# Kernel optimization log

Measured on AMD Instinct MI355X. Metric: run time of the kernel, lower is better.

The kernel has to match this reference:

```python
import jax, jax.numpy as jnp
import numpy as np

NEG_INF = -9e15  # matches torch's -9000000000000000.0 mask value


def setup_inputs() -> dict:
    key = jax.random.key(0)
    k1, k2, k3, k4 = jax.random.split(key, 4)
    B, F_in, T, N, F_out = 8, 64, 12, 512, 64
    inp = {
        "input": jax.random.normal(k1, (B, F_in, T, N), dtype=jnp.float32),
        "adj": jax.random.randint(k2, (B, T, N, N), 0, 2, dtype=jnp.int32),
        "W": jax.random.normal(k3, (F_in, F_out), dtype=jnp.float32),
        "a": jax.random.normal(k4, (2 * F_out, 1), dtype=jnp.float32),
    }
    return inp


def reference(input, adj, W, a):
    # input: [B, F_in, T, N], adj: [B, T, N, N]
    F_out = W.shape[1]
    x = jnp.transpose(input, (0, 2, 3, 1))          # [B, T, N, F_in]
    Wh = jnp.einsum('btnf,fo->btno', x, W)          # [B, T, N, F_out]
    # score decomposition: e[i,j] = leakyrelu(a1.Wh_i + a2.Wh_j)
    a1 = a[:F_out, 0]
    a2 = a[F_out:, 0]
    f1 = Wh @ a1                                    # [B, T, N]
    f2 = Wh @ a2                                    # [B, T, N]
    e = jax.nn.leaky_relu(f1[..., :, None] + f2[..., None, :], 0.2)
    e = jnp.where(adj > 0, e, NEG_INF)
    attn = jax.nn.softmax(e, axis=-1)               # [B, T, N, N]
    h = jnp.einsum('btij,btjo->btio', attn, Wh)     # [B, T, N, F_out]
    return jax.nn.elu(h)                            # concat=True -> elu
```

## Files before the change

kernel.cpp:

```cpp
#include <hip/hip_runtime.h>
#include <hip/hip_bf16.h>

typedef float fx4 __attribute__((ext_vector_type(4)));
typedef short i16x8 __attribute__((ext_vector_type(8)));
typedef unsigned short u16;

#define NEG_INF_F (-9.0e15f)

__device__ inline u16 f2bf(float v){
  __hip_bfloat16 h = __float2bfloat16(v);
  return *reinterpret_cast<u16*>(&h);
}

__global__ __launch_bounds__(256) void gat_prep(
    const float* __restrict__ input,
    const float* __restrict__ W,
    const float* __restrict__ Avec,
    u16*   __restrict__ whB,
    float* __restrict__ f1w,
    float* __restrict__ f2w)
{
  __shared__ float Wl[64*64];
  __shared__ float Al[128];
  __shared__ u16   Rp[16384];
  const int tid = threadIdx.x;
  const int bt  = blockIdx.y;
  const int b   = bt / 12, t = bt % 12;
  const int xb  = blockIdx.x;
  const int n   = xb * 256 + tid;

  {
    const fx4* src = (const fx4*)W;
    fx4* dst = (fx4*)Wl;
    #pragma unroll
    for (int i = 0; i < 4; ++i) dst[tid + 256*i] = src[tid + 256*i];
    if (tid < 32) ((fx4*)Al)[tid] = ((const fx4*)Avec)[tid];
  }
  __syncthreads();

  const float* xp = input + ((size_t)b*64*12 + t) * 512 + n;

  fx4 acc[16];
  #pragma unroll
  for (int i = 0; i < 16; ++i) acc[i] = (fx4){0.f,0.f,0.f,0.f};

  #pragma unroll 8
  for (int f = 0; f < 64; ++f) {
    float xv = xp[(size_t)f * 6144];
    const fx4* wr = (const fx4*)(Wl + f*64);
    #pragma unroll
    for (int o4 = 0; o4 < 16; ++o4) acc[o4] += xv * wr[o4];
  }

  float s1 = 0.f, s2 = 0.f;
  #pragma unroll
  for (int o4 = 0; o4 < 16; ++o4) {
    fx4 v  = acc[o4];
    fx4 w1 = ((const fx4*)Al)[o4];
    fx4 w2 = ((const fx4*)Al)[o4 + 16];
    s1 += v[0]*w1[0] + v[1]*w1[1] + v[2]*w1[2] + v[3]*w1[3];
    s2 += v[0]*w2[0] + v[1]*w2[1] + v[2]*w2[2] + v[3]*w2[3];
  }
  f1w[bt*512 + n] = s1;
  f2w[bt*512 + n] = s2;

  const int ktl  = (n >> 5) & 7;
  const int q    = (n >> 3) & 3;
  const int e    = n & 7;
  const int rowb = ktl*2048 + q*128 + e;
  #pragma unroll
  for (int o4 = 0; o4 < 16; ++o4) {
    #pragma unroll
    for (int c = 0; c < 4; ++c) {
      const int o = o4*4 + c;
      Rp[rowb + (o >> 4)*512 + (o & 15)*8] = f2bf(acc[o4][c]);
    }
  }
  __syncthreads();

  uint4* dst = (uint4*)(whB + ((size_t)bt*16 + xb*8) * 2048);
  const uint4* src = (const uint4*)Rp;
  #pragma unroll
  for (int i = 0; i < 8; ++i) dst[tid + 256*i] = src[tid + 256*i];
}

__global__ __launch_bounds__(256, 4) void gat_attn(
    const int*   __restrict__ adj,
    const u16*   __restrict__ whB,
    const float* __restrict__ f1w,
    const float* __restrict__ f2w,
    float*       __restrict__ out)
{
  __shared__ float f2l[512];
  __shared__ float f1l[16];
  __shared__ float wmax[4];
  __shared__ float sums[16];
  __shared__ u16   attnl[16*512];

  const int tid = threadIdx.x;
  const int l   = tid & 63;
  const int w   = tid >> 6;
  const int bt  = blockIdx.y;
  const int it  = blockIdx.x;

  float2 fv = ((const float2*)(f2w + bt*512))[tid];
  ((float2*)f2l)[tid] = fv;
  float m2 = fmaxf(fv.x, fv.y);
  #pragma unroll
  for (int off = 32; off >= 1; off >>= 1) m2 = fmaxf(m2, __shfl_xor(m2, off));
  if (l == 0) wmax[w] = m2;
  if (tid < 16) f1l[tid] = f1w[bt*512 + it*16 + tid];
  __syncthreads();
  const float F2max = fmaxf(fmaxf(wmax[0], wmax[1]), fmaxf(wmax[2], wmax[3]));

  const fx4 f20 = ((const fx4*)f2l)[l];
  const fx4 f21 = ((const fx4*)f2l)[64 + l];
  fx4 v0, v1, vh0, vh1;
  #pragma unroll
  for (int c = 0; c < 4; ++c) {
    v0[c]  = __expf(f20[c] - F2max);
    v1[c]  = __expf(f21[c] - F2max);
    vh0[c] = __expf(0.2f*(f20[c] - F2max));
    vh1[c] = __expf(0.2f*(f21[c] - F2max));
  }

  const int R0     = w * 4;
  const int row_g0 = it*16 + R0;
  const int4* adj4 = (const int4*)(adj + (size_t)bt*512*512);

  int4 pre[2][2];
  #pragma unroll
  for (int p = 0; p < 2; ++p) {
    const int4* ar = adj4 + (size_t)(row_g0 + p) * 128;
    pre[p][0] = ar[l];
    pre[p][1] = ar[64 + l];
  }

  float ssum[4];
  #pragma unroll
  for (int r = 0; r < 4; ++r) {
    const int4 c0 = pre[r & 1][0];
    const int4 c1 = pre[r & 1][1];
    if (r + 2 < 4) {
      const int4* ar = adj4 + (size_t)(row_g0 + r + 2) * 128;
      pre[r & 1][0] = ar[l];
      pre[r & 1][1] = ar[64 + l];
    }
    const float f1v = f1l[R0 + r];

    float mx = NEG_INF_F;
    mx = fmaxf(mx, (c0.x > 0) ? f20[0] : NEG_INF_F);
    mx = fmaxf(mx, (c0.y > 0) ? f20[1] : NEG_INF_F);
    mx = fmaxf(mx, (c0.z > 0) ? f20[2] : NEG_INF_F);
    mx = fmaxf(mx, (c0.w > 0) ? f20[3] : NEG_INF_F);
    mx = fmaxf(mx, (c1.x > 0) ? f21[0] : NEG_INF_F);
    mx = fmaxf(mx, (c1.y > 0) ? f21[1] : NEG_INF_F);
    mx = fmaxf(mx, (c1.z > 0) ? f21[2] : NEG_INF_F);
    mx = fmaxf(mx, (c1.w > 0) ? f21[3] : NEG_INF_F);
    #pragma unroll
    for (int off = 32; off >= 1; off >>= 1) mx = fmaxf(mx, __shfl_xor(mx, off));

    const float tM = f1v + mx;
    const float M  = fmaxf(tM, 0.2f*tM);
    const float gap = F2max - mx;

    float sum = 0.f;
    ushort4 pk0, pk1;
    if (gap <= 80.f) {
      const float u  = __expf(f1v + F2max - M);
      const float uh = __expf(0.2f*(f1v + F2max) - M);
      const float thr = -f1v;
      float pv;
#define GAT_F(pkf, cc, ff, vv, vvh) { \
      const bool cpos = (ff) > thr; \
      float a = cpos ? (vv) : (vvh); \
      float bb = cpos ? u : uh; \
      pv = ((cc) > 0) ? a*bb : 0.f; sum += pv; pkf = f2bf(pv); }
      GAT_F(pk0.x, c0.x, f20[0], v0[0], vh0[0])
      GAT_F(pk0.y, c0.y, f20[1], v0[1], vh0[1])
      GAT_F(pk0.z, c0.z, f20[2], v0[2], vh0[2])
      GAT_F(pk0.w, c0.w, f20[3], v0[3], vh0[3])
      GAT_F(pk1.x, c1.x, f21[0], v1[0], vh1[0])
      GAT_F(pk1.y, c1.y, f21[1], v1[1], vh1[1])
      GAT_F(pk1.z, c1.z, f21[2], v1[2], vh1[2])
      GAT_F(pk1.w, c1.w, f21[3], v1[3], vh1[3])
#undef GAT_F
    } else {
      const float Mf = (mx == NEG_INF_F) ? NEG_INF_F : M;
      float pv;
#define GAT_S(pkf, cc, ff) { float s = f1v + (ff); float lr = fmaxf(s, 0.2f*s); \
      float ee = ((cc) > 0) ? lr : NEG_INF_F; \
      pv = __expf(ee - Mf); sum += pv; pkf = f2bf(pv); }
      GAT_S(pk0.x, c0.x, f20[0]) GAT_S(pk0.y, c0.y, f20[1])
      GAT_S(pk0.z, c0.z, f20[2]) GAT_S(pk0.w, c0.w, f20[3])
      GAT_S(pk1.x, c1.x, f21[0]) GAT_S(pk1.y, c1.y, f21[1])
      GAT_S(pk1.z, c1.z, f21[2]) GAT_S(pk1.w, c1.w, f21[3])
#undef GAT_S
    }
    ssum[r] = sum;

    const int rowR = R0 + r;
    const unsigned swz = (unsigned)((rowR & 7) << 4);
    char* base = (char*)attnl + rowR * 1024;
    *(ushort4*)(base + (((unsigned)(      8*l)) ^ swz)) = pk0;
    *(ushort4*)(base + (((unsigned)(512 + 8*l)) ^ swz)) = pk1;
  }

  #pragma unroll
  for (int r = 0; r < 4; ++r) {
    #pragma unroll
    for (int off = 32; off >= 1; off >>= 1) ssum[r] += __shfl_xor(ssum[r], off);
  }
  if (l == 0) {
    #pragma unroll
    for (int r = 0; r < 4; ++r) sums[R0 + r] = ssum[r];
  }
  __syncthreads();

  const int r = l & 15, q = l >> 4;
  const int ct = w;
  const unsigned swzB = (unsigned)((r & 7) << 4);
  const char* aBase = (const char*)attnl + r * 1024;
  const u16*  wp    = whB + (size_t)bt*32768 + ct*512 + l*8;
  fx4 acc = {0,0,0,0};

  #pragma unroll
  for (int kt = 0; kt < 16; ++kt) {
    i16x8 af = *(const i16x8*)(aBase + (((unsigned)(kt*64 + q*16)) ^ swzB));
    i16x8 bf = *(const i16x8*)(wp + kt*2048);
    acc = __builtin_amdgcn_mfma_f32_16x16x32_bf16(af, bf, acc, 0, 0, 0);
  }

  float* op = out + ((size_t)bt*512 + it*16) * 64;
  #pragma unroll
  for (int rr = 0; rr < 4; ++rr) {
    const float rs = 1.0f / sums[q*4 + rr];
    float v = acc[rr] * rs;
    v = v > 0.f ? v : expm1f(v);
    op[(q*4 + rr)*64 + ct*16 + r] = v;
  }
}

extern "C" void kernel_launch(void* const* d_in, const int* in_sizes, int n_in,
                              void* d_out, int out_size, void* d_ws, size_t ws_size,
                              hipStream_t stream) {
  const float* input = (const float*)d_in[0];
  const int*   adj   = (const int*)  d_in[1];
  const float* W     = (const float*)d_in[2];
  const float* Avec  = (const float*)d_in[3];
  float* out = (float*)d_out;

  char* ws = (char*)d_ws;
  u16*   whB = (u16*)ws;
  float* f1w = (float*)(ws + 6291456);
  float* f2w = (float*)(ws + 6291456 + 196608);

  gat_prep<<<dim3(2, 96), 256, 0, stream>>>(input, W, Avec, whB, f1w, f2w);
  gat_attn<<<dim3(32, 96), 256, 0, stream>>>(adj, whB, f1w, f2w, out);
}
```

Before: 50.62 us.

## Process two 16-row tiles per block with early adj prefetch and XCD-aware remap

Each attention block now covers 32 rows as two 16-row tiles. All adjacency loads for the first tile are issued at kernel start, before the f2 reduction. The second tile's adjacency is prefetched while the first tile's MFMA phase runs. A flat 1536-block grid is remapped so consecutive block ids spread across the 8 XCDs while neighbouring tiles of the same batch/time slice stay together. This halves per-block setup (f2 load, max, exp tables) and is meant to hide adj latency, at the cost of more registers and fewer blocks in flight.

```diff
diff --git a/kernel.cpp b/kernel.cpp
--- a/kernel.cpp
+++ b/kernel.cpp
@@ -92,26 +92,41 @@
     float*       __restrict__ out)
 {
   __shared__ float f2l[512];
-  __shared__ float f1l[16];
-  __shared__ float wmax[4];
-  __shared__ float sums[16];
+  __shared__ float f1l[32];
+  __shared__ float wmaxl[4];
+  __shared__ float sums[2][16];
   __shared__ u16   attnl[16*512];
 
   const int tid = threadIdx.x;
   const int l   = tid & 63;
   const int w   = tid >> 6;
-  const int bt  = blockIdx.y;
-  const int it  = blockIdx.x;
+
+  const int id  = blockIdx.x;
+  const int sid = (id & 7) * 192 + (id >> 3);
+  const int bt  = sid >> 4;
+  const int it  = sid & 15;
+
+  const int4* adj4 = (const int4*)(adj + (size_t)bt*512*512);
+
+  const int grow0 = it*32 + w*4;
+  int4 p0[4][2];
+  #pragma unroll
+  for (int r = 0; r < 4; ++r) {
+    const int4* ar = adj4 + (size_t)(grow0 + r) * 128;
+    p0[r][0] = ar[l];
+    p0[r][1] = ar[64 + l];
+  }
+  __builtin_amdgcn_sched_barrier(0);
 
   float2 fv = ((const float2*)(f2w + bt*512))[tid];
   ((float2*)f2l)[tid] = fv;
   float m2 = fmaxf(fv.x, fv.y);
   #pragma unroll
   for (int off = 32; off >= 1; off >>= 1) m2 = fmaxf(m2, __shfl_xor(m2, off));
-  if (l == 0) wmax[w] = m2;
-  if (tid < 16) f1l[tid] = f1w[bt*512 + it*16 + tid];
-  __syncthreads();
-  const float F2max = fmaxf(fmaxf(wmax[0], wmax[1]), fmaxf(wmax[2], wmax[3]));
+  if (l == 0) wmaxl[w] = m2;
+  if (tid < 32) f1l[tid] = f1w[bt*512 + it*32 + tid];
+  __syncthreads();
+  const float F2max = fmaxf(fmaxf(wmaxl[0], wmaxl[1]), fmaxf(wmaxl[2], wmaxl[3]));
 
   const fx4 f20 = ((const fx4*)f2l)[l];
   const fx4 f21 = ((const fx4*)f2l)[64 + l];
@@ -124,121 +139,127 @@
     vh1[c] = __expf(0.2f*(f21[c] - F2max));
   }
 
-  const int R0     = w * 4;
-  const int row_g0 = it*16 + R0;
-  const int4* adj4 = (const int4*)(adj + (size_t)bt*512*512);
-
-  int4 pre[2][2];
-  #pragma unroll
-  for (int p = 0; p < 2; ++p) {
-    const int4* ar = adj4 + (size_t)(row_g0 + p) * 128;
-    pre[p][0] = ar[l];
-    pre[p][1] = ar[64 + l];
-  }
-
-  float ssum[4];
+#define PHASE_A(pre, tId)                                                    \
+  {                                                                          \
+    float ssum[4];                                                           \
+    _Pragma("unroll")                                                        \
+    for (int r = 0; r < 4; ++r) {                                            \
+      const int4 c0 = pre[r][0];                                             \
+      const int4 c1 = pre[r][1];                                             \
+      const float f1v = f1l[(tId)*16 + w*4 + r];                             \
+      float mx = NEG_INF_F;                                                  \
+      mx = fmaxf(mx, (c0.x > 0) ? f20[0] : NEG_INF_F);                       \
+      mx = fmaxf(mx, (c0.y > 0) ? f20[1] : NEG_INF_F);                       \
+      mx = fmaxf(mx, (c0.z > 0) ? f20[2] : NEG_INF_F);                       \
+      mx = fmaxf(mx, (c0.w > 0) ? f20[3] : NEG_INF_F);                       \
+      mx = fmaxf(mx, (c1.x > 0) ? f21[0] : NEG_INF_F);                       \
+      mx = fmaxf(mx, (c1.y > 0) ? f21[1] : NEG_INF_F);                       \
+      mx = fmaxf(mx, (c1.z > 0) ? f21[2] : NEG_INF_F);                       \
+      mx = fmaxf(mx, (c1.w > 0) ? f21[3] : NEG_INF_F);                       \
+      _Pragma("unroll")                                                      \
+      for (int off = 32; off >= 1; off >>= 1)                                \
+        mx = fmaxf(mx, __shfl_xor(mx, off));                                 \
+      const float tM = f1v + mx;                                             \
+      const float M  = fmaxf(tM, 0.2f*tM);                                   \
+      const float gap = F2max - mx;                                          \
+      float sum = 0.f;                                                       \
+      ushort4 pk0, pk1;                                                      \
+      if (gap <= 80.f) {                                                     \
+        const float u   = __expf(f1v + F2max - M);                           \
+        const float uh  = __expf(0.2f*(f1v + F2max) - M);                    \
+        const float thr = -f1v;                                              \
+        float pv;                                                            \
+        GAT_F(pk0.x, c0.x, f20[0], v0[0], vh0[0])                            \
+        GAT_F(pk0.y, c0.y, f20[1], v0[1], vh0[1])                            \
+        GAT_F(pk0.z, c0.z, f20[2], v0[2], vh0[2])                            \
+        GAT_F(pk0.w, c0.w, f20[3], v0[3], vh0[3])                            \
+        GAT_F(pk1.x, c1.x, f21[0], v1[0], vh1[0])                            \
+        GAT_F(pk1.y, c1.y, f21[1], v1[1], vh1[1])                            \
+        GAT_F(pk1.z, c1.z, f21[2], v1[2], vh1[2])                            \
+        GAT_F(pk1.w, c1.w, f21[3], v1[3], vh1[3])                            \
+      } else {                                                               \
+        const float Mf = (mx == NEG_INF_F) ? NEG_INF_F : M;                  \
+        float pv;                                                            \
+        GAT_S(pk0.x, c0.x, f20[0]) GAT_S(pk0.y, c0.y, f20[1])                \
+        GAT_S(pk0.z, c0.z, f20[2]) GAT_S(pk0.w, c0.w, f20[3])                \
+        GAT_S(pk1.x, c1.x, f21[0]) GAT_S(pk1.y, c1.y, f21[1])                \
+        GAT_S(pk1.z, c1.z, f21[2]) GAT_S(pk1.w, c1.w, f21[3])                \
+      }                                                                      \
+      ssum[r] = sum;                                                         \
+      const int rowR = w*4 + r;                                              \
+      const unsigned swz = (unsigned)((rowR & 7) << 4);                      \
+      char* base = (char*)attnl + rowR * 1024;                               \
+      *(ushort4*)(base + (((unsigned)(      8*l)) ^ swz)) = pk0;             \
+      *(ushort4*)(base + (((unsigned)(512 + 8*l)) ^ swz)) = pk1;             \
+    }                                                                        \
+    _Pragma("unroll")                                                        \
+    for (int r = 0; r < 4; ++r) {                                            \
+      _Pragma("unroll")                                                      \
+      for (int off = 32; off >= 1; off >>= 1)                                \
+        ssum[r] += __shfl_xor(ssum[r], off);                                 \
+    }                                                                        \
+    if (l == 0) {                                                            \
+      _Pragma("unroll")                                                      \
+      for (int r = 0; r < 4; ++r) sums[tId][w*4 + r] = ssum[r];              \
+    }                                                                        \
+  }
+
+#define GAT_F(pkf, cc, ff, vv, vvh) {                                        \
+      const bool cpos = (ff) > thr;                                          \
+      float a = cpos ? (vv) : (vvh);                                         \
+      float bb = cpos ? u : uh;                                              \
+      pv = ((cc) > 0) ? a*bb : 0.f; sum += pv; pkf = f2bf(pv); }
+#define GAT_S(pkf, cc, ff) { float s = f1v + (ff); float lr = fmaxf(s, 0.2f*s); \
+      float ee = ((cc) > 0) ? lr : NEG_INF_F;                                \
+      pv = __expf(ee - Mf); sum += pv; pkf = f2bf(pv); }
+
+#define PHASE_B(tId)                                                         \
+  {                                                                          \
+    const int r = l & 15, q = l >> 4;                                        \
+    const unsigned swzB = (unsigned)((r & 7) << 4);                          \
+    const char* aBase = (const char*)attnl + r * 1024;                       \
+    const u16*  wp    = whB + (size_t)bt*32768 + w*512 + l*8;                \
+    fx4 acc = {0,0,0,0};                                                     \
+    _Pragma("unroll")                                                        \
+    for (int kt = 0; kt < 16; ++kt) {                                        \
+      i16x8 af = *(const i16x8*)(aBase + (((unsigned)(kt*64 + q*16)) ^ swzB)); \
+      i16x8 bf = *(const i16x8*)(wp + kt*2048);                              \
+      acc = __builtin_amdgcn_mfma_f32_16x16x32_bf16(af, bf, acc, 0, 0, 0);   \
+    }                                                                        \
+    float* op = out + ((size_t)bt*512 + it*32 + (tId)*16) * 64;              \
+    _Pragma("unroll")                                                        \
+    for (int rr = 0; rr < 4; ++rr) {                                         \
+      const float rs = 1.0f / sums[tId][q*4 + rr];                           \
+      float v = acc[rr] * rs;                                                \
+      v = v > 0.f ? v : expm1f(v);                                           \
+      op[(q*4 + rr)*64 + w*16 + r] = v;                                      \
+    }                                                                        \
+  }
+
+  PHASE_A(p0, 0)
+
+  const int grow1 = it*32 + 16 + w*4;
+  int4 p1[4][2];
   #pragma unroll
   for (int r = 0; r < 4; ++r) {
-    const int4 c0 = pre[r & 1][0];
-    const int4 c1 = pre[r & 1][1];
-    if (r + 2 < 4) {
-      const int4* ar = adj4 + (size_t)(row_g0 + r + 2) * 128;
-      pre[r & 1][0] = ar[l];
-      pre[r & 1][1] = ar[64 + l];
-    }
-    const float f1v = f1l[R0 + r];
-
-    float mx = NEG_INF_F;
-    mx = fmaxf(mx, (c0.x > 0) ? f20[0] : NEG_INF_F);
-    mx = fmaxf(mx, (c0.y > 0) ? f20[1] : NEG_INF_F);
-    mx = fmaxf(mx, (c0.z > 0) ? f20[2] : NEG_INF_F);
-    mx = fmaxf(mx, (c0.w > 0) ? f20[3] : NEG_INF_F);
-    mx = fmaxf(mx, (c1.x > 0) ? f21[0] : NEG_INF_F);
-    mx = fmaxf(mx, (c1.y > 0) ? f21[1] : NEG_INF_F);
-    mx = fmaxf(mx, (c1.z > 0) ? f21[2] : NEG_INF_F);
-    mx = fmaxf(mx, (c1.w > 0) ? f21[3] : NEG_INF_F);
-    #pragma unroll
-    for (int off = 32; off >= 1; off >>= 1) mx = fmaxf(mx, __shfl_xor(mx, off));
-
-    const float tM = f1v + mx;
-    const float M  = fmaxf(tM, 0.2f*tM);
-    const float gap = F2max - mx;
-
-    float sum = 0.f;
-    ushort4 pk0, pk1;
-    if (gap <= 80.f) {
-      const float u  = __expf(f1v + F2max - M);
-      const float uh = __expf(0.2f*(f1v + F2max) - M);
-      const float thr = -f1v;
-      float pv;
-#define GAT_F(pkf, cc, ff, vv, vvh) { \
-      const bool cpos = (ff) > thr; \
-      float a = cpos ? (vv) : (vvh); \
-      float bb = cpos ? u : uh; \
-      pv = ((cc) > 0) ? a*bb : 0.f; sum += pv; pkf = f2bf(pv); }
-      GAT_F(pk0.x, c0.x, f20[0], v0[0], vh0[0])
-      GAT_F(pk0.y, c0.y, f20[1], v0[1], vh0[1])
-      GAT_F(pk0.z, c0.z, f20[2], v0[2], vh0[2])
-      GAT_F(pk0.w, c0.w, f20[3], v0[3], vh0[3])
-      GAT_F(pk1.x, c1.x, f21[0], v1[0], vh1[0])
-      GAT_F(pk1.y, c1.y, f21[1], v1[1], vh1[1])
-      GAT_F(pk1.z, c1.z, f21[2], v1[2], vh1[2])
-      GAT_F(pk1.w, c1.w, f21[3], v1[3], vh1[3])
+    const int4* ar = adj4 + (size_t)(grow1 + r) * 128;
+    p1[r][0] = ar[l];
+    p1[r][1] = ar[64 + l];
+  }
+  __builtin_amdgcn_sched_barrier(0);
+
+  __syncthreads();
+  PHASE_B(0)
+  __syncthreads();
+
+  PHASE_A(p1, 1)
+  __syncthreads();
+  PHASE_B(1)
+
+#undef PHASE_A
+#undef PHASE_B
 #undef GAT_F
-    } else {
-      const float Mf = (mx == NEG_INF_F) ? NEG_INF_F : M;
-      float pv;
-#define GAT_S(pkf, cc, ff) { float s = f1v + (ff); float lr = fmaxf(s, 0.2f*s); \
-      float ee = ((cc) > 0) ? lr : NEG_INF_F; \
-      pv = __expf(ee - Mf); sum += pv; pkf = f2bf(pv); }
-      GAT_S(pk0.x, c0.x, f20[0]) GAT_S(pk0.y, c0.y, f20[1])
-      GAT_S(pk0.z, c0.z, f20[2]) GAT_S(pk0.w, c0.w, f20[3])
-      GAT_S(pk1.x, c1.x, f21[0]) GAT_S(pk1.y, c1.y, f21[1])
-      GAT_S(pk1.z, c1.z, f21[2]) GAT_S(pk1.w, c1.w, f21[3])
 #undef GAT_S
-    }
-    ssum[r] = sum;
-
-    const int rowR = R0 + r;
-    const unsigned swz = (unsigned)((rowR & 7) << 4);
-    char* base = (char*)attnl + rowR * 1024;
-    *(ushort4*)(base + (((unsigned)(      8*l)) ^ swz)) = pk0;
-    *(ushort4*)(base + (((unsigned)(512 + 8*l)) ^ swz)) = pk1;
-  }
-
-  #pragma unroll
-  for (int r = 0; r < 4; ++r) {
-    #pragma unroll
-    for (int off = 32; off >= 1; off >>= 1) ssum[r] += __shfl_xor(ssum[r], off);
-  }
-  if (l == 0) {
-    #pragma unroll
-    for (int r = 0; r < 4; ++r) sums[R0 + r] = ssum[r];
-  }
-  __syncthreads();
-
-  const int r = l & 15, q = l >> 4;
-  const int ct = w;
-  const unsigned swzB = (unsigned)((r & 7) << 4);
-  const char* aBase = (const char*)attnl + r * 1024;
-  const u16*  wp    = whB + (size_t)bt*32768 + ct*512 + l*8;
-  fx4 acc = {0,0,0,0};
-
-  #pragma unroll
-  for (int kt = 0; kt < 16; ++kt) {
-    i16x8 af = *(const i16x8*)(aBase + (((unsigned)(kt*64 + q*16)) ^ swzB));
-    i16x8 bf = *(const i16x8*)(wp + kt*2048);
-    acc = __builtin_amdgcn_mfma_f32_16x16x32_bf16(af, bf, acc, 0, 0, 0);
-  }
-
-  float* op = out + ((size_t)bt*512 + it*16) * 64;
-  #pragma unroll
-  for (int rr = 0; rr < 4; ++rr) {
-    const float rs = 1.0f / sums[q*4 + rr];
-    float v = acc[rr] * rs;
-    v = v > 0.f ? v : expm1f(v);
-    op[(q*4 + rr)*64 + ct*16 + r] = v;
-  }
 }
 
 extern "C" void kernel_launch(void* const* d_in, const int* in_sizes, int n_in,
@@ -256,5 +277,5 @@
   float* f2w = (float*)(ws + 6291456 + 196608);
 
   gat_prep<<<dim3(2, 96), 256, 0, stream>>>(input, W, Avec, whB, f1w, f2w);
-  gat_attn<<<dim3(32, 96), 256, 0, stream>>>(adj, whB, f1w, f2w, out);
-}
+  gat_attn<<<1536, 256, 0, stream>>>(adj, whB, f1w, f2w, out);
+}
```

Result: slower. 53.96 us (+6.6%).

## Precompress adjacency matrix into bitmask in a separate kernel before attention

Applied to the files above, without the earlier changes.

Adds a kernel that reads the int32 adjacency once and packs it into 32-bit bitmasks, and the attention kernel loads the compact mask into shared memory instead of streaming int4 adjacency rows. This is meant to decouple the bandwidth-heavy adjacency read from the compute-heavy softmax/MFMA stage. It adds an extra launch and a serialized pass over the full adjacency, and removes the overlap of adjacency loads with compute.

```diff
diff --git a/kernel.cpp b/kernel.cpp
--- a/kernel.cpp
+++ b/kernel.cpp
@@ -10,6 +10,25 @@
 __device__ inline u16 f2bf(float v){
   __hip_bfloat16 h = __float2bfloat16(v);
   return *reinterpret_cast<u16*>(&h);
+}
+
+__global__ __launch_bounds__(256) void gat_compress(
+    const int* __restrict__ adj, unsigned* __restrict__ maskw)
+{
+  const int t = blockIdx.x * 256 + threadIdx.x;
+  const uint4* src = (const uint4*)adj + (size_t)t * 8;
+  uint4 v[8];
+  #pragma unroll
+  for (int i = 0; i < 8; ++i) v[i] = src[i];
+  unsigned m = 0u;
+  #pragma unroll
+  for (int i = 0; i < 8; ++i) {
+    if ((int)v[i].x > 0) m |= 1u << (4*i+0);
+    if ((int)v[i].y > 0) m |= 1u << (4*i+1);
+    if ((int)v[i].z > 0) m |= 1u << (4*i+2);
+    if ((int)v[i].w > 0) m |= 1u << (4*i+3);
+  }
+  maskw[t] = m;
 }
 
 __global__ __launch_bounds__(256) void gat_prep(
@@ -85,7 +104,7 @@
 }
 
 __global__ __launch_bounds__(256, 4) void gat_attn(
-    const int*   __restrict__ adj,
+    const unsigned* __restrict__ maskw,
     const u16*   __restrict__ whB,
     const float* __restrict__ f1w,
     const float* __restrict__ f2w,
@@ -93,8 +112,9 @@
 {
   __shared__ float f2l[512];
   __shared__ float f1l[16];
-  __shared__ float wmax[4];
+  __shared__ float wmaxl[4];
   __shared__ float sums[16];
+  __shared__ unsigned maskl[16][16];
   __shared__ u16   attnl[16*512];
 
   const int tid = threadIdx.x;
@@ -103,15 +123,16 @@
   const int bt  = blockIdx.y;
   const int it  = blockIdx.x;
 
+  ((unsigned*)maskl)[tid] = maskw[((size_t)bt*512 + it*16)*16 + tid];
   float2 fv = ((const float2*)(f2w + bt*512))[tid];
   ((float2*)f2l)[tid] = fv;
   float m2 = fmaxf(fv.x, fv.y);
   #pragma unroll
   for (int off = 32; off >= 1; off >>= 1) m2 = fmaxf(m2, __shfl_xor(m2, off));
-  if (l == 0) wmax[w] = m2;
+  if (l == 0) wmaxl[w] = m2;
   if (tid < 16) f1l[tid] = f1w[bt*512 + it*16 + tid];
   __syncthreads();
-  const float F2max = fmaxf(fmaxf(wmax[0], wmax[1]), fmaxf(wmax[2], wmax[3]));
+  const float F2max = fmaxf(fmaxf(wmaxl[0], wmaxl[1]), fmaxf(wmaxl[2], wmaxl[3]));
 
   const fx4 f20 = ((const fx4*)f2l)[l];
   const fx4 f21 = ((const fx4*)f2l)[64 + l];
@@ -124,39 +145,27 @@
     vh1[c] = __expf(0.2f*(f21[c] - F2max));
   }
 
-  const int R0     = w * 4;
-  const int row_g0 = it*16 + R0;
-  const int4* adj4 = (const int4*)(adj + (size_t)bt*512*512);
-
-  int4 pre[2][2];
-  #pragma unroll
-  for (int p = 0; p < 2; ++p) {
-    const int4* ar = adj4 + (size_t)(row_g0 + p) * 128;
-    pre[p][0] = ar[l];
-    pre[p][1] = ar[64 + l];
-  }
+  const int R0 = w * 4;
+  const int wi = l >> 3;
+  const int sh = (l & 7) * 4;
 
   float ssum[4];
   #pragma unroll
   for (int r = 0; r < 4; ++r) {
-    const int4 c0 = pre[r & 1][0];
-    const int4 c1 = pre[r & 1][1];
-    if (r + 2 < 4) {
-      const int4* ar = adj4 + (size_t)(row_g0 + r + 2) * 128;
-      pre[r & 1][0] = ar[l];
-      pre[r & 1][1] = ar[64 + l];
-    }
-    const float f1v = f1l[R0 + r];
+    const int rowR = R0 + r;
+    const unsigned nib0 = (maskl[rowR][wi]     >> sh) & 0xFu;
+    const unsigned nib1 = (maskl[rowR][8 + wi] >> sh) & 0xFu;
+    const float f1v = f1l[rowR];
 
     float mx = NEG_INF_F;
-    mx = fmaxf(mx, (c0.x > 0) ? f20[0] : NEG_INF_F);
-    mx = fmaxf(mx, (c0.y > 0) ? f20[1] : NEG_INF_F);
-    mx = fmaxf(mx, (c0.z > 0) ? f20[2] : NEG_INF_F);
-    mx = fmaxf(mx, (c0.w > 0) ? f20[3] : NEG_INF_F);
-    mx = fmaxf(mx, (c1.x > 0) ? f21[0] : NEG_INF_F);
-    mx = fmaxf(mx, (c1.y > 0) ? f21[1] : NEG_INF_F);
-    mx = fmaxf(mx, (c1.z > 0) ? f21[2] : NEG_INF_F);
-    mx = fmaxf(mx, (c1.w > 0) ? f21[3] : NEG_INF_F);
+    mx = fmaxf(mx, (nib0 & 1u) ? f20[0] : NEG_INF_F);
+    mx = fmaxf(mx, (nib0 & 2u) ? f20[1] : NEG_INF_F);
+    mx = fmaxf(mx, (nib0 & 4u) ? f20[2] : NEG_INF_F);
+    mx = fmaxf(mx, (nib0 & 8u) ? f20[3] : NEG_INF_F);
+    mx = fmaxf(mx, (nib1 & 1u) ? f21[0] : NEG_INF_F);
+    mx = fmaxf(mx, (nib1 & 2u) ? f21[1] : NEG_INF_F);
+    mx = fmaxf(mx, (nib1 & 4u) ? f21[2] : NEG_INF_F);
+    mx = fmaxf(mx, (nib1 & 8u) ? f21[3] : NEG_INF_F);
     #pragma unroll
     for (int off = 32; off >= 1; off >>= 1) mx = fmaxf(mx, __shfl_xor(mx, off));
 
@@ -171,35 +180,34 @@
       const float uh = __expf(0.2f*(f1v + F2max) - M);
       const float thr = -f1v;
       float pv;
-#define GAT_F(pkf, cc, ff, vv, vvh) { \
+#define GAT_F(pkf, bb_, ff, vv, vvh) { \
       const bool cpos = (ff) > thr; \
       float a = cpos ? (vv) : (vvh); \
       float bb = cpos ? u : uh; \
-      pv = ((cc) > 0) ? a*bb : 0.f; sum += pv; pkf = f2bf(pv); }
-      GAT_F(pk0.x, c0.x, f20[0], v0[0], vh0[0])
-      GAT_F(pk0.y, c0.y, f20[1], v0[1], vh0[1])
-      GAT_F(pk0.z, c0.z, f20[2], v0[2], vh0[2])
-      GAT_F(pk0.w, c0.w, f20[3], v0[3], vh0[3])
-      GAT_F(pk1.x, c1.x, f21[0], v1[0], vh1[0])
-      GAT_F(pk1.y, c1.y, f21[1], v1[1], vh1[1])
-      GAT_F(pk1.z, c1.z, f21[2], v1[2], vh1[2])
-      GAT_F(pk1.w, c1.w, f21[3], v1[3], vh1[3])
+      pv = (bb_) ? a*bb : 0.f; sum += pv; pkf = f2bf(pv); }
+      GAT_F(pk0.x, nib0 & 1u, f20[0], v0[0], vh0[0])
+      GAT_F(pk0.y, nib0 & 2u, f20[1], v0[1], vh0[1])
+      GAT_F(pk0.z, nib0 & 4u, f20[2], v0[2], vh0[2])
+      GAT_F(pk0.w, nib0 & 8u, f20[3], v0[3], vh0[3])
+      GAT_F(pk1.x, nib1 & 1u, f21[0], v1[0], vh1[0])
+      GAT_F(pk1.y, nib1 & 2u, f21[1], v1[1], vh1[1])
+      GAT_F(pk1.z, nib1 & 4u, f21[2], v1[2], vh1[2])
+      GAT_F(pk1.w, nib1 & 8u, f21[3], v1[3], vh1[3])
 #undef GAT_F
     } else {
       const float Mf = (mx == NEG_INF_F) ? NEG_INF_F : M;
       float pv;
-#define GAT_S(pkf, cc, ff) { float s = f1v + (ff); float lr = fmaxf(s, 0.2f*s); \
-      float ee = ((cc) > 0) ? lr : NEG_INF_F; \
+#define GAT_S(pkf, bb_, ff) { float s = f1v + (ff); float lr = fmaxf(s, 0.2f*s); \
+      float ee = (bb_) ? lr : NEG_INF_F; \
       pv = __expf(ee - Mf); sum += pv; pkf = f2bf(pv); }
-      GAT_S(pk0.x, c0.x, f20[0]) GAT_S(pk0.y, c0.y, f20[1])
-      GAT_S(pk0.z, c0.z, f20[2]) GAT_S(pk0.w, c0.w, f20[3])
-      GAT_S(pk1.x, c1.x, f21[0]) GAT_S(pk1.y, c1.y, f21[1])
-      GAT_S(pk1.z, c1.z, f21[2]) GAT_S(pk1.w, c1.w, f21[3])
+      GAT_S(pk0.x, nib0 & 1u, f20[0]) GAT_S(pk0.y, nib0 & 2u, f20[1])
+      GAT_S(pk0.z, nib0 & 4u, f20[2]) GAT_S(pk0.w, nib0 & 8u, f20[3])
+      GAT_S(pk1.x, nib1 & 1u, f21[0]) GAT_S(pk1.y, nib1 & 2u, f21[1])
+      GAT_S(pk1.z, nib1 & 4u, f21[2]) GAT_S(pk1.w, nib1 & 8u, f21[3])
 #undef GAT_S
     }
     ssum[r] = sum;
 
-    const int rowR = R0 + r;
     const unsigned swz = (unsigned)((rowR & 7) << 4);
     char* base = (char*)attnl + rowR * 1024;
     *(ushort4*)(base + (((unsigned)(      8*l)) ^ swz)) = pk0;
@@ -251,10 +259,12 @@
   float* out = (float*)d_out;
 
   char* ws = (char*)d_ws;
-  u16*   whB = (u16*)ws;
-  float* f1w = (float*)(ws + 6291456);
-  float* f2w = (float*)(ws + 6291456 + 196608);
-
+  u16*      whB   = (u16*)ws;
+  float*    f1w   = (float*)(ws + 6291456);
+  float*    f2w   = (float*)(ws + 6291456 + 196608);
+  unsigned* maskw = (unsigned*)(ws + 6291456 + 393216);
+
+  gat_compress<<<3072, 256, 0, stream>>>(adj, maskw);
   gat_prep<<<dim3(2, 96), 256, 0, stream>>>(input, W, Avec, whB, f1w, f2w);
-  gat_attn<<<dim3(32, 96), 256, 0, stream>>>(adj, whB, f1w, f2w, out);
-}
+  gat_attn<<<dim3(32, 96), 256, 0, stream>>>(maskw, whB, f1w, f2w, out);
+}
```

Result: slower. 56.54 us (+11.7%).
